# Kernel optimization log

Hardware: AMD Instinct MI355X
Metric: run time of the kernel (lower is better)

The kernel has to match this reference:

```python
import jax, jax.numpy as jnp
import numpy as np

B, H, W = 2, 224, 224
E, NH, DH, DFF = 64, 4, 16, 2048


def _conv2d(x, w, b):
    # stride-1 3x3 conv, padding=1 == SAME
    y = jax.lax.conv_general_dilated(x, w, (1, 1), 'SAME',
                                     dimension_numbers=('NCHW', 'OIHW', 'NCHW'))
    return y + b[None, :, None, None]


def _layer_norm(x, g, b, eps=1e-5):
    mu = x.mean(-1, keepdims=True)
    xc = x - mu
    var = (xc * xc).mean(-1, keepdims=True)
    return g * xc * jax.lax.rsqrt(var + eps) + b


def setup_inputs() -> dict:
    key = jax.random.key(0)
    ks = jax.random.split(key, 16)
    rn = lambda k, shape, s=0.05: jax.random.normal(k, shape, dtype=jnp.float32) * s
    z = lambda n: jnp.zeros((n,), jnp.float32)
    return {
        'x': jax.random.normal(ks[0], (B, 3, H, W), dtype=jnp.float32),
        'enc_w1': rn(ks[1], (64, 3, 3, 3)), 'enc_b1': z(64),
        'enc_w2': rn(ks[2], (64, 64, 3, 3)), 'enc_b2': z(64),
        'in_proj_w': rn(ks[3], (3 * E, E)), 'in_proj_b': z(3 * E),
        'out_proj_w': rn(ks[4], (E, E)), 'out_proj_b': z(E),
        'ln1_g': jnp.ones((E,), jnp.float32), 'ln1_b': z(E),
        'ffn_w1': rn(ks[5], (DFF, E)), 'ffn_b1': z(DFF),
        'ffn_w2': rn(ks[6], (E, DFF)), 'ffn_b2': z(E),
        'ln2_g': jnp.ones((E,), jnp.float32), 'ln2_b': z(E),
        'sf_w1': rn(ks[7], (32, 64, 3, 3)), 'sf_b1': z(32),
        'sf_w2': rn(ks[8], (9, 32, 3, 3)), 'sf_b2': z(9),
        'dec_w1': rn(ks[9], (64, 1, 3, 3)), 'dec_b1': z(64),
        'dec_w2': rn(ks[10], (1, 64, 3, 3)), 'dec_b2': z(1),
    }


def _forward(x, enc_w1, enc_b1, enc_w2, enc_b2,
             in_proj_w, in_proj_b, out_proj_w, out_proj_b,
             ln1_g, ln1_b, ffn_w1, ffn_b1, ffn_w2, ffn_b2, ln2_g, ln2_b,
             sf_w1, sf_b1, sf_w2, sf_b2, dec_w1, dec_b1, dec_w2, dec_b2):
    # ---- encoder ----
    e = jax.nn.relu(_conv2d(x, enc_w1, enc_b1))
    e = jax.nn.relu(_conv2d(e, enc_w2, enc_b2))
    b, c, h, w = e.shape
    # torch TransformerEncoderLayer default batch_first=False: [B, HW, E] is (S=B, N=HW, E)
    t = e.reshape(b, c, h * w).transpose(0, 2, 1)  # [S=B, N=HW, E]
    qkv = t @ in_proj_w.T + in_proj_b
    q, k, v = jnp.split(qkv, 3, axis=-1)
    S, N = q.shape[0], q.shape[1]
    q = q.reshape(S, N, NH, DH)
    k = k.reshape(S, N, NH, DH)
    v = v.reshape(S, N, NH, DH)
    scores = jnp.einsum('snhd,tnhd->nhst', q, k) / np.float32(np.sqrt(DH))
    attn = jnp.einsum('nhst,tnhd->snhd', jax.nn.softmax(scores, axis=-1), v)
    attn = attn.reshape(S, N, E) @ out_proj_w.T + out_proj_b
    t = _layer_norm(t + attn, ln1_g, ln1_b)
    ff = jax.nn.relu(t @ ffn_w1.T + ffn_b1) @ ffn_w2.T + ffn_b2
    t = _layer_norm(t + ff, ln2_g, ln2_b)
    enc2 = t.transpose(0, 2, 1).reshape(b, c, h, w)
    # ---- spatially adaptive per-pixel 3x3 filter (KPN-style) ----
    f = _conv2d(_conv2d(enc2, sf_w1, sf_b1), sf_w2, sf_b2)
    filters = f.reshape(b, 3, 3, h, w)  # per-pixel 3x3 kernel
    s = x.sum(axis=1)  # accumulate over the 3 input channels -> [B,H,W]
    sp = jnp.pad(s, ((0, 0), (1, 1), (1, 1)))
    patches = jnp.stack([sp[:, u:u + h, v:v + w] for u in range(3) for v in range(3)],
                        axis=1).reshape(b, 3, 3, h, w)
    fused = (filters * patches).sum(axis=(1, 2))[:, None]  # [B,1,H,W]
    # ---- decoder ----
    d = jax.nn.relu(_conv2d(fused, dec_w1, dec_b1))
    return jax.nn.sigmoid(_conv2d(d, dec_w2, dec_b2))


def reference(x, enc_w1, enc_b1, enc_w2, enc_b2,
              in_proj_w, in_proj_b, out_proj_w, out_proj_b,
              ln1_g, ln1_b, ffn_w1, ffn_b1, ffn_w2, ffn_b2, ln2_g, ln2_b,
              sf_w1, sf_b1, sf_w2, sf_b2, dec_w1, dec_b1, dec_w2, dec_b2):
    return _forward(x, enc_w1, enc_b1, enc_w2, enc_b2,
                    in_proj_w, in_proj_b, out_proj_w, out_proj_b,
                    ln1_g, ln1_b, ffn_w1, ffn_b1, ffn_w2, ffn_b2, ln2_g, ln2_b,
                    sf_w1, sf_b1, sf_w2, sf_b2, dec_w1, dec_b1, dec_w2, dec_b2)
```

## Files before the change

kernel.cpp:

```cpp
#include <hip/hip_runtime.h>
#include <hip/hip_bf16.h>
#include <cstddef>

#define HW   50176
#define NPIX 100352
#define IW   224

typedef unsigned short ushort_t;
typedef __attribute__((ext_vector_type(8))) short bf16x8;
typedef __attribute__((ext_vector_type(8))) unsigned short ushort8;
typedef __attribute__((ext_vector_type(4))) float f32x4;
typedef __attribute__((ext_vector_type(2))) _Float16 f16x2;
typedef __attribute__((ext_vector_type(8))) _Float16 f16x8;

__device__ inline ushort_t f2bf(float f) {
    __hip_bfloat16 h = __float2bfloat16(f);
    return __builtin_bit_cast(ushort_t, h);
}
__device__ inline float bf2f(ushort_t u) {
    return __uint_as_float(((unsigned)u) << 16);
}
__device__ inline bf16x8 ldg8(const ushort_t* p) {
    return *reinterpret_cast<const bf16x8*>(p);
}
__device__ inline void b2f8(const ushort_t* p, float* f) {
    ushort8 v = *reinterpret_cast<const ushort8*>(p);
#pragma unroll
    for (int i = 0; i < 8; i++) f[i] = bf2f(v[i]);
}
__device__ inline f16x2 pk16(float a, float b) {
    return __builtin_bit_cast(f16x2, __builtin_amdgcn_cvt_pkrtz(a, b));
}

__device__ inline void dma16(const ushort_t* g, ushort_t* l) {
    __builtin_amdgcn_global_load_lds(
        (const __attribute__((address_space(1))) void*)g,
        (__attribute__((address_space(3))) void*)l, 16, 0, 0);
}

__device__ void conv1_body(int gid, const float* __restrict__ x,
                           const float* __restrict__ w,
                           const float* __restrict__ bias,
                           ushort_t* __restrict__ out)
{
    int b = gid >= HW;
    int p = gid - b * HW;
    int y = p / IW, xx = p - y * IW;

    float v[27];
#pragma unroll
    for (int ci = 0; ci < 3; ci++) {
        const float* ip = x + ((size_t)(b * 3 + ci)) * HW;
#pragma unroll
        for (int t = 0; t < 9; t++) {
            int dy = t / 3 - 1, dx = t % 3 - 1;
            int yy = y + dy, xc = xx + dx;
            float tv = 0.f;
            if ((unsigned)yy < (unsigned)IW && (unsigned)xc < (unsigned)IW)
                tv = ip[yy * IW + xc];
            v[ci * 9 + t] = tv;
        }
    }
#pragma unroll
    for (int g = 0; g < 8; g++) {
        ushort8 o8;
#pragma unroll
        for (int i = 0; i < 8; i++) {
            int co = g * 8 + i;
            float a = bias[co];
            const float* wp = w + co * 27;
#pragma unroll
            for (int k = 0; k < 27; k++) a = fmaf(v[k], wp[k], a);
            o8[i] = f2bf(fmaxf(a, 0.f));
        }
        *reinterpret_cast<ushort8*>(out + (size_t)gid * 64 + g * 8) = o8;
    }
}

__global__ __launch_bounds__(256) void prep_conv1_k(
    const float* __restrict__ x,     const float* __restrict__ enc_w1,
    const float* __restrict__ enc_b1, ushort_t* __restrict__ E1b,
    const float* __restrict__ in_w,  ushort_t* __restrict__ in_wb,
    const float* __restrict__ out_w, ushort_t* __restrict__ out_wb,
    const float* __restrict__ w1,    ushort_t* __restrict__ w1p,
    const float* __restrict__ w2,    _Float16* __restrict__ w2s,
    const float* __restrict__ ec2,   ushort_t* __restrict__ wc2p,
    const float* __restrict__ s1,    ushort_t* __restrict__ ws1p,
    const float* __restrict__ s2,    ushort_t* __restrict__ ws2)
{
    if (blockIdx.x < 392) {
        conv1_body(blockIdx.x * 256 + threadIdx.x, x, enc_w1, enc_b1, E1b);
        return;
    }
    int idx = (blockIdx.x - 392) * 256 + threadIdx.x;
    if (idx < 12288) { in_wb[idx] = f2bf(in_w[idx]); return; }
    idx -= 12288;
    if (idx < 4096)  { out_wb[idx] = f2bf(out_w[idx]); return; }
    idx -= 4096;
    if (idx < 131072){
        int j = idx >> 6, e = idx & 63;
        int c = j >> 6, jl = j & 63;
        w1p[(size_t)c * 6144 + jl * 72 + e] = f2bf(w1[idx]);
        return;
    }
    idx -= 131072;
    if (idx < 131072){
        int j    = idx & 7;
        int lane = (idx >> 3) & 63;
        int rest = idx >> 9;
        int nt   = rest & 3;
        int cp   = rest >> 2;
        int p    = cp & 1;
        int c    = cp >> 1;
        int quad = lane >> 4;
        int e2   = nt * 16 + (lane & 15);
        int hl   = (j < 4) ? (quad * 4 + j) : (16 + quad * 4 + (j - 4));
        int hidden = c * 64 + p * 32 + hl;
        w2s[idx] = (_Float16)w2[(size_t)e2 * 2048 + hidden];
        return;
    }
    idx -= 131072;
    if (idx < 36864) {
        int ci = idx & 63, co = (idx >> 6) & 63, t = idx >> 12;
        wc2p[(size_t)t * 4608 + co * 72 + ci] = f2bf(ec2[((size_t)co * 64 + ci) * 9 + t]);
        return;
    }
    idx -= 36864;
    if (idx < 18432) {
        int ci = idx & 63, co = (idx >> 6) & 31, t = idx >> 11;
        ws1p[(size_t)t * 2560 + co * 72 + ci] = f2bf(s1[((size_t)co * 64 + ci) * 9 + t]);
        return;
    }
    idx -= 18432;
    if (idx < 4608)  {
        int ci = idx % 32;
        int t  = (idx / 32) % 9;
        int co = idx / 288;
        ws2[idx] = (co < 9) ? f2bf(s2[((size_t)co * 32 + ci) * 9 + t]) : (ushort_t)0;
        return;
    }
}

__global__ __launch_bounds__(256) void enc2xf_k(
    const ushort_t* __restrict__ E1b, const ushort_t* __restrict__ Wc2p,
    const float* __restrict__ enc_b2,
    const ushort_t* __restrict__ Wqkv, const float* __restrict__ Bqkv,
    const ushort_t* __restrict__ Wo, const float* __restrict__ Bo,
    const float* __restrict__ g, const float* __restrict__ be,
    ushort_t* __restrict__ T1b)
{
    __shared__ ushort_t Q[128 * 200];
    __shared__ ushort_t WT[9216];

    int tid = threadIdx.x, wave = tid >> 6, lane = tid & 63;
    int lm = lane & 15, quad = lane >> 4;
    int p0 = blockIdx.x * 64;

    {
        int lr0 = wave * 32;
        int m[2], py[2], px[2];
#pragma unroll
        for (int mt = 0; mt < 2; mt++) {
            int lr = lr0 + mt * 16 + lm;
            int gp = p0 + (lr & 63);
            m[mt] = (lr >> 6) * HW + gp;
            py[mt] = gp / IW;
            px[mt] = gp - py[mt] * IW;
        }

        f32x4 acc[2][4] = {};
        bf16x8 zz = {};

        auto dma_tap = [&](int t, int pb) {
            const ushort_t* gw = Wc2p + (size_t)t * 4608;
#pragma unroll
            for (int i = 0; i < 3; i++) {
                int idx = i * 4 + wave;
                if (idx < 9)
                    dma16(gw + idx * 512 + lane * 8, &WT[pb * 4608 + idx * 512]);
            }
        };

        dma_tap(0, 0);

        for (int t = 0; t < 9; t++) {
            int pb = t & 1;
            __syncthreads();
            if (t < 8) dma_tap(t + 1, pb ^ 1);

            int dy = t / 3 - 1, dx = t % 3 - 1;
            bf16x8 af[2][2];
#pragma unroll
            for (int mt = 0; mt < 2; mt++) {
                bool ok = (unsigned)(py[mt] + dy) < (unsigned)IW &&
                          (unsigned)(px[mt] + dx) < (unsigned)IW;
                const ushort_t* ip = E1b + (size_t)(m[mt] + dy * IW + dx) * 64 + quad * 8;
#pragma unroll
                for (int ks = 0; ks < 2; ks++)
                    af[mt][ks] = ok ? ldg8(ip + ks * 32) : zz;
            }
#pragma unroll
            for (int nt = 0; nt < 4; nt++) {
                const ushort_t* wp = &WT[pb * 4608 + (nt * 16 + lm) * 72 + quad * 8];
#pragma unroll
                for (int ks = 0; ks < 2; ks++) {
                    bf16x8 bfv = *reinterpret_cast<const bf16x8*>(wp + ks * 32);
#pragma unroll
                    for (int mt = 0; mt < 2; mt++)
                        acc[mt][nt] = __builtin_amdgcn_mfma_f32_16x16x32_bf16(
                            af[mt][ks], bfv, acc[mt][nt], 0, 0, 0);
                }
            }
        }

        __syncthreads();
#pragma unroll
        for (int nt = 0; nt < 4; nt++) {
            float bv = enc_b2[nt * 16 + lm];
#pragma unroll
            for (int mt = 0; mt < 2; mt++)
#pragma unroll
                for (int r = 0; r < 4; r++) {
                    int lr = lr0 + mt * 16 + quad * 4 + r;
                    WT[lr * 72 + nt * 16 + lm] =
                        f2bf(fmaxf(acc[mt][nt][r] + bv, 0.f));
                }
        }
    }
    __syncthreads();

#pragma unroll
    for (int mt = 0; mt < 2; mt++) {
        int lA = mt * 64 + wave * 16;
        bf16x8 a[2];
#pragma unroll
        for (int ks = 0; ks < 2; ks++)
            a[ks] = *reinterpret_cast<const bf16x8*>(
                &WT[(lA + lm) * 72 + ks * 32 + quad * 8]);
        f32x4 acc[12] = {};
#pragma unroll
        for (int nt = 0; nt < 12; nt++)
#pragma unroll
            for (int ks = 0; ks < 2; ks++) {
                bf16x8 b = ldg8(Wqkv + (size_t)(nt * 16 + lm) * 64 + ks * 32 + quad * 8);
                acc[nt] = __builtin_amdgcn_mfma_f32_16x16x32_bf16(a[ks], b, acc[nt], 0, 0, 0);
            }
        int lrow = lA + quad * 4;
#pragma unroll
        for (int nt = 0; nt < 12; nt++) {
            float bb = Bqkv[nt * 16 + lm];
#pragma unroll
            for (int r = 0; r < 4; r++)
                Q[(lrow + r) * 200 + nt * 16 + lm] = f2bf(acc[nt][r] + bb);
        }
    }
    __syncthreads();

    {
        int px = tid >> 2, h = tid & 3;
        ushort_t* r0 = &Q[px * 200 + h * 16];
        ushort_t* r1 = &Q[(64 + px) * 200 + h * 16];

        float q0[16], k0[16], v0[16], q1[16], k1[16], v1[16];
        b2f8(r0,       q0); b2f8(r0 + 8,   q0 + 8);
        b2f8(r0 + 64,  k0); b2f8(r0 + 72,  k0 + 8);
        b2f8(r0 + 128, v0); b2f8(r0 + 136, v0 + 8);
        b2f8(r1,       q1); b2f8(r1 + 8,   q1 + 8);
        b2f8(r1 + 64,  k1); b2f8(r1 + 72,  k1 + 8);
        b2f8(r1 + 128, v1); b2f8(r1 + 136, v1 + 8);

        float s00 = 0, s01 = 0, s10 = 0, s11 = 0;
#pragma unroll
        for (int d = 0; d < 16; d++) {
            s00 += q0[d] * k0[d]; s01 += q0[d] * k1[d];
            s10 += q1[d] * k0[d]; s11 += q1[d] * k1[d];
        }
        s00 *= 0.25f; s01 *= 0.25f; s10 *= 0.25f; s11 *= 0.25f;

        float m0 = fmaxf(s00, s01);
        float e00 = __expf(s00 - m0), e01 = __expf(s01 - m0);
        float i0 = 1.f / (e00 + e01);
        float p00 = e00 * i0, p01 = e01 * i0;

        float m1 = fmaxf(s10, s11);
        float e10 = __expf(s10 - m1), e11 = __expf(s11 - m1);
        float i1 = 1.f / (e10 + e11);
        float p10 = e10 * i1, p11 = e11 * i1;

#pragma unroll
        for (int c = 0; c < 2; c++) {
            ushort8 a0v, a1v;
#pragma unroll
            for (int i = 0; i < 8; i++) {
                int d = c * 8 + i;
                a0v[i] = f2bf(p00 * v0[d] + p01 * v1[d]);
                a1v[i] = f2bf(p10 * v0[d] + p11 * v1[d]);
            }
            *reinterpret_cast<ushort8*>(r0 + c * 8) = a0v;
            *reinterpret_cast<ushort8*>(r1 + c * 8) = a1v;
        }
    }
    __syncthreads();

#pragma unroll
    for (int mt = 0; mt < 2; mt++) {
        int lA = mt * 64 + wave * 16;
        size_t gbase = (size_t)((mt == 0 ? p0 : HW + p0) + wave * 16);
        bf16x8 a[2];
#pragma unroll
        for (int ks = 0; ks < 2; ks++)
            a[ks] = *reinterpret_cast<const bf16x8*>(
                &Q[(lA + lm) * 200 + ks * 32 + quad * 8]);
        f32x4 acc[4] = {};
#pragma unroll
        for (int nt = 0; nt < 4; nt++)
#pragma unroll
            for (int ks = 0; ks < 2; ks++) {
                bf16x8 b = ldg8(Wo + (size_t)(nt * 16 + lm) * 64 + ks * 32 + quad * 8);
                acc[nt] = __builtin_amdgcn_mfma_f32_16x16x32_bf16(a[ks], b, acc[nt], 0, 0, 0);
            }

        float bv[4], gv[4], bev[4];
#pragma unroll
        for (int nt = 0; nt < 4; nt++) {
            bv[nt]  = Bo[nt * 16 + lm];
            gv[nt]  = g[nt * 16 + lm];
            bev[nt] = be[nt * 16 + lm];
        }
#pragma unroll
        for (int r = 0; r < 4; r++) {
            int lr = lA + quad * 4 + r;
            size_t row = gbase + quad * 4 + r;
            float v[4]; float s = 0.f;
#pragma unroll
            for (int nt = 0; nt < 4; nt++) {
                v[nt] = acc[nt][r] + bv[nt] + bf2f(WT[lr * 72 + nt * 16 + lm]);
                s += v[nt];
            }
#pragma unroll
            for (int o = 8; o; o >>= 1) s += __shfl_xor(s, o, 64);
            float mu = s * 0.015625f;
            float q = 0.f;
#pragma unroll
            for (int nt = 0; nt < 4; nt++) { v[nt] -= mu; q += v[nt] * v[nt]; }
#pragma unroll
            for (int o = 8; o; o >>= 1) q += __shfl_xor(q, o, 64);
            float rstd = rsqrtf(q * 0.015625f + 1e-5f);
#pragma unroll
            for (int nt = 0; nt < 4; nt++)
                T1b[row * 64 + nt * 16 + lm] = f2bf(gv[nt] * v[nt] * rstd + bev[nt]);
        }
    }
}

template<int KS, int NT, int TAPUS, int NISSUE, int ACT, bool WF32, bool WB16>
__global__ __launch_bounds__(256) void neconv_lds_k(
    const ushort_t* __restrict__ In, const ushort_t* __restrict__ Wp,
    const float* __restrict__ bias, float* __restrict__ Of,
    ushort_t* __restrict__ Ob)
{
    const int CIN = KS * 32, LDO = NT * 16;
    __shared__ ushort_t Wl[2][TAPUS];

    int tid = threadIdx.x, wave = tid >> 6, lane = tid & 63;
    int lm = lane & 15, quad = lane >> 4;
    int m0 = blockIdx.x * 128 + wave * 32;

    int m[2], py[2], px[2];
#pragma unroll
    for (int mt = 0; mt < 2; mt++) {
        int mm = m0 + mt * 16 + lm;
        m[mt] = mm;
        int p = mm - (mm >= HW ? HW : 0);
        py[mt] = p / IW;
        px[mt] = p - py[mt] * IW;
    }

    f32x4 acc[2][NT] = {};
    bf16x8 zz = {};

    auto dma_tap = [&](int t, int pb) {
        const ushort_t* g = Wp + (size_t)t * TAPUS;
#pragma unroll
        for (int i = 0; i < (NISSUE + 3) / 4; i++) {
            int idx = i * 4 + wave;
            if (idx < NISSUE)
                dma16(g + idx * 512 + lane * 8, &Wl[pb][idx * 512]);
        }
    };

    dma_tap(0, 0);

    for (int t = 0; t < 9; t++) {
        int pb = t & 1;
        __syncthreads();
        if (t < 8) dma_tap(t + 1, pb ^ 1);

        int dy = t / 3 - 1, dx = t % 3 - 1;
        bf16x8 af[2][KS];
#pragma unroll
        for (int mt = 0; mt < 2; mt++) {
            bool ok = (unsigned)(py[mt] + dy) < (unsigned)IW &&
                      (unsigned)(px[mt] + dx) < (unsigned)IW;
            const ushort_t* ip = In + (size_t)(m[mt] + dy * IW + dx) * CIN + quad * 8;
#pragma unroll
            for (int ks = 0; ks < KS; ks++)
                af[mt][ks] = ok ? ldg8(ip + ks * 32) : zz;
        }
#pragma unroll
        for (int nt = 0; nt < NT; nt++) {
            const ushort_t* wp = &Wl[pb][(nt * 16 + lm) * 72 + quad * 8];
#pragma unroll
            for (int ks = 0; ks < KS; ks++) {
                bf16x8 bfv = *reinterpret_cast<const bf16x8*>(wp + ks * 32);
#pragma unroll
                for (int mt = 0; mt < 2; mt++)
                    acc[mt][nt] = __builtin_amdgcn_mfma_f32_16x16x32_bf16(
                        af[mt][ks], bfv, acc[mt][nt], 0, 0, 0);
            }
        }
    }

#pragma unroll
    for (int nt = 0; nt < NT; nt++) {
        int col = nt * 16 + lm;
        float bv = bias[col];
#pragma unroll
        for (int mt = 0; mt < 2; mt++)
#pragma unroll
            for (int r = 0; r < 4; r++) {
                int row = m0 + mt * 16 + quad * 4 + r;
                float v = acc[mt][nt][r] + bv;
                if (ACT) v = fmaxf(v, 0.f);
                if (WF32) Of[(size_t)row * LDO + col] = v;
                if (WB16) Ob[(size_t)row * LDO + col] = f2bf(v);
            }
    }
}

__global__ __launch_bounds__(512) void ffn9_k(
    const ushort_t* __restrict__ T1b,
    const ushort_t* __restrict__ W1p, const float* __restrict__ B1,
    const _Float16* __restrict__ W2s, const float* __restrict__ B2,
    const float* __restrict__ g, const float* __restrict__ be,
    ushort_t* __restrict__ OutTb)
{
    __shared__ ushort_t W1lds[3][6144];
    __shared__ ushort_t W2lds[3][4096];
    __shared__ float    B1l[2048];

    int tid = threadIdx.x, wave = tid >> 6, lane = tid & 63;
    int lm = lane & 15, quad = lane >> 4;
    int rowbase = blockIdx.x * 256 + wave * 32;

    *reinterpret_cast<float4*>(&B1l[tid * 4]) =
        *reinterpret_cast<const float4*>(B1 + tid * 4);

    bf16x8 Bt[2][2];
#pragma unroll
    for (int mt = 0; mt < 2; mt++)
#pragma unroll
        for (int ks = 0; ks < 2; ks++)
            Bt[mt][ks] = ldg8(T1b + (size_t)(rowbase + mt * 16 + lm) * 64 + ks * 32 + quad * 8);

    __syncthreads();

    auto dma_chunk = [&](int c, int pb) {
        const ushort_t* g1 = W1p + (size_t)c * 6144;
        const ushort_t* g2 = (const ushort_t*)(W2s + (size_t)c * 4096);
#pragma unroll
        for (int i = 0; i < 3; i++) {
            int idx = i * 8 + wave;
            if (idx < 12)
                dma16(g1 + idx * 512 + lane * 8, &W1lds[pb][idx * 512]);
            else if (idx < 20)
                dma16(g2 + (idx - 12) * 512 + lane * 8,
                      &W2lds[pb][(idx - 12) * 512]);
        }
    };

    dma_chunk(0, 0);
    dma_chunk(1, 1);

    f32x4 acc[2][4] = {};

    for (int c = 0; c < 32; c++) {
        int pb = c % 3;

        if (c < 31) {
            if (wave < 4) asm volatile("s_waitcnt vmcnt(3)" ::: "memory");
            else          asm volatile("s_waitcnt vmcnt(2)" ::: "memory");
        } else {
            asm volatile("s_waitcnt vmcnt(0)" ::: "memory");
        }
        __builtin_amdgcn_s_barrier();
        asm volatile("" ::: "memory");

        if (c + 2 < 32) dma_chunk(c + 2, (c + 2) % 3);

        const ushort_t* w1l = &W1lds[pb][0];
        const ushort_t* w2l = &W2lds[pb][0];

#pragma unroll
        for (int p = 0; p < 2; p++) {
            bf16x8 w1r[2][2];
            f16x8  w2r[4];
            float4 b1r[2];
#pragma unroll
            for (int s = 0; s < 2; s++) {
                int ul = p * 2 + s;
#pragma unroll
                for (int ks = 0; ks < 2; ks++)
                    w1r[s][ks] = *reinterpret_cast<const bf16x8*>(
                        &w1l[(ul * 16 + lm) * 72 + ks * 32 + quad * 8]);
                b1r[s] = *reinterpret_cast<const float4*>(
                    &B1l[(c * 4 + ul) * 16 + quad * 4]);
            }
#pragma unroll
            for (int nt = 0; nt < 4; nt++)
                w2r[nt] = *reinterpret_cast<const f16x8*>(
                    &w2l[((p * 4 + nt) * 64 + lane) * 8]);

            f32x4 h[2][2];
#pragma unroll
            for (int s = 0; s < 2; s++) {
                f32x4 binit = {b1r[s].x, b1r[s].y, b1r[s].z, b1r[s].w};
#pragma unroll
                for (int mt = 0; mt < 2; mt++) h[s][mt] = binit;
            }

            __builtin_amdgcn_s_setprio(1);
#pragma unroll
            for (int s = 0; s < 2; s++)
#pragma unroll
                for (int ks = 0; ks < 2; ks++)
#pragma unroll
                    for (int mt = 0; mt < 2; mt++)
                        h[s][mt] = __builtin_amdgcn_mfma_f32_16x16x32_bf16(
                            w1r[s][ks], Bt[mt][ks], h[s][mt], 0, 0, 0);

            f16x8 aH[2];
#pragma unroll
            for (int mt = 0; mt < 2; mt++) {
                f16x2 t0 = pk16(fmaxf(h[0][mt][0], 0.f), fmaxf(h[0][mt][1], 0.f));
                f16x2 t1 = pk16(fmaxf(h[0][mt][2], 0.f), fmaxf(h[0][mt][3], 0.f));
                f16x2 t2 = pk16(fmaxf(h[1][mt][0], 0.f), fmaxf(h[1][mt][1], 0.f));
                f16x2 t3 = pk16(fmaxf(h[1][mt][2], 0.f), fmaxf(h[1][mt][3], 0.f));
                f16x8 a;
                a[0] = t0[0]; a[1] = t0[1]; a[2] = t1[0]; a[3] = t1[1];
                a[4] = t2[0]; a[5] = t2[1]; a[6] = t3[0]; a[7] = t3[1];
                aH[mt] = a;
            }

#pragma unroll
            for (int nt = 0; nt < 4; nt++)
#pragma unroll
                for (int mt = 0; mt < 2; mt++)
                    acc[mt][nt] = __builtin_amdgcn_mfma_f32_16x16x32_f16(
                        aH[mt], w2r[nt], acc[mt][nt], 0, 0, 0);
            __builtin_amdgcn_s_setprio(0);
        }
    }

    float b2v[4], gv[4], bev[4];
#pragma unroll
    for (int nt = 0; nt < 4; nt++) {
        b2v[nt] = B2[nt * 16 + lm];
        gv[nt]  = g[nt * 16 + lm];
        bev[nt] = be[nt * 16 + lm];
    }
#pragma unroll
    for (int mt = 0; mt < 2; mt++)
#pragma unroll
        for (int r = 0; r < 4; r++) {
            int row = rowbase + mt * 16 + quad * 4 + r;
            float v[4]; float s = 0.f;
#pragma unroll
            for (int nt = 0; nt < 4; nt++) {
                v[nt] = acc[mt][nt][r] + b2v[nt] +
                        bf2f(T1b[(size_t)row * 64 + nt * 16 + lm]);
                s += v[nt];
            }
#pragma unroll
            for (int o = 8; o; o >>= 1) s += __shfl_xor(s, o, 64);
            float mu = s * 0.015625f;
            float q = 0.f;
#pragma unroll
            for (int nt = 0; nt < 4; nt++) { v[nt] -= mu; q += v[nt] * v[nt]; }
#pragma unroll
            for (int o = 8; o; o >>= 1) q += __shfl_xor(q, o, 64);
            float rstd = rsqrtf(q * 0.015625f + 1e-5f);
#pragma unroll
            for (int nt = 0; nt < 4; nt++)
                OutTb[(size_t)row * 64 + nt * 16 + lm] =
                    f2bf(gv[nt] * v[nt] * rstd + bev[nt]);
        }
}

__global__ __launch_bounds__(256) void sf2kpn_k(
    const ushort_t* __restrict__ In,
    const ushort_t* __restrict__ Wsw,
    const float* __restrict__ bias,
    const float* __restrict__ x,
    float* __restrict__ fused)
{
    __shared__ float Fl[128 * 12];
    int tid = threadIdx.x, wave = tid >> 6, lane = tid & 63;
    int lm = lane & 15, quad = lane >> 4;
    int m0 = blockIdx.x * 128 + wave * 32;

    int m[2], py[2], px[2];
#pragma unroll
    for (int mt = 0; mt < 2; mt++) {
        int mm = m0 + mt * 16 + lm;
        m[mt] = mm;
        int p = mm - (mm >= HW ? HW : 0);
        py[mt] = p / IW;
        px[mt] = p - py[mt] * IW;
    }

    f32x4 acc[2] = {};
    bf16x8 zz = {};

#pragma unroll 3
    for (int t = 0; t < 9; t++) {
        int dy = t / 3 - 1, dx = t % 3 - 1;
        bf16x8 af[2];
#pragma unroll
        for (int mt = 0; mt < 2; mt++) {
            bool ok = (unsigned)(py[mt] + dy) < (unsigned)IW &&
                      (unsigned)(px[mt] + dx) < (unsigned)IW;
            af[mt] = ok ? ldg8(In + (size_t)(m[mt] + dy * IW + dx) * 32 + quad * 8) : zz;
        }
        bf16x8 bfv = ldg8(Wsw + ((size_t)lm * 9 + t) * 32 + quad * 8);
#pragma unroll
        for (int mt = 0; mt < 2; mt++)
            acc[mt] = __builtin_amdgcn_mfma_f32_16x16x32_bf16(af[mt], bfv, acc[mt], 0, 0, 0);
    }

    if (lm < 9) {
        float bv = bias[lm];
#pragma unroll
        for (int mt = 0; mt < 2; mt++)
#pragma unroll
            for (int r = 0; r < 4; r++) {
                int lrow = wave * 32 + mt * 16 + quad * 4 + r;
                Fl[lrow * 12 + lm] = acc[mt][r] + bv;
            }
    }
    __syncthreads();

    if (tid < 128) {
        int gid = blockIdx.x * 128 + tid;
        int b = gid >= HW;
        int p = gid - b * HW;
        int y = p / IW, xx = p - y * IW;
        const float* fp = &Fl[tid * 12];
        const float* xp = x + (size_t)b * 3 * HW;
        float a = 0.f;
#pragma unroll
        for (int u = 0; u < 3; u++) {
            int yy = y + u - 1;
            if ((unsigned)yy >= (unsigned)IW) continue;
#pragma unroll
            for (int v = 0; v < 3; v++) {
                int xc = xx + v - 1;
                if ((unsigned)xc >= (unsigned)IW) continue;
                int o = yy * IW + xc;
                float s = xp[o] + xp[HW + o] + xp[2 * HW + o];
                a += fp[u * 3 + v] * s;
            }
        }
        fused[gid] = a;
    }
}

__global__ __launch_bounds__(256) void dec_fused_k(
    const float* __restrict__ fused,
    const float* __restrict__ w1, const float* __restrict__ b1,
    const float* __restrict__ w2, const float* __restrict__ b2,
    float* __restrict__ out)
{
    int gid = blockIdx.x * 256 + threadIdx.x;
    int b = gid >= HW;
    int p = gid - b * HW;
    int y = p / IW, xx = p - y * IW;
    const float* ip = fused + (size_t)b * HW;

    float F[25];
#pragma unroll
    for (int u = 0; u < 5; u++)
#pragma unroll
        for (int v = 0; v < 5; v++) {
            int yy = y + u - 2, xc = xx + v - 2;
            float t = 0.f;
            if ((unsigned)yy < (unsigned)IW && (unsigned)xc < (unsigned)IW)
                t = ip[yy * IW + xc];
            F[u * 5 + v] = t;
        }
    float nm[9];
#pragma unroll
    for (int n = 0; n < 9; n++) {
        int yy = y + n / 3 - 1, xc = xx + n % 3 - 1;
        nm[n] = ((unsigned)yy < (unsigned)IW && (unsigned)xc < (unsigned)IW) ? 1.f : 0.f;
    }

    float acc = b2[0];
    for (int c = 0; c < 64; c++) {
        float w1c[9], w2c[9];
#pragma unroll
        for (int s = 0; s < 9; s++) { w1c[s] = w1[c * 9 + s]; w2c[s] = w2[c * 9 + s]; }
        float bc = b1[c];
#pragma unroll
        for (int n = 0; n < 9; n++) {
            int ny = n / 3, nx0 = n % 3;
            float h = bc;
#pragma unroll
            for (int s = 0; s < 9; s++)
                h = fmaf(F[(ny + s / 3) * 5 + (nx0 + s % 3)], w1c[s], h);
            acc = fmaf(fmaxf(h, 0.f), w2c[n] * nm[n], acc);
        }
    }
    out[gid] = 1.f / (1.f + __expf(-acc));
}

extern "C" void kernel_launch(void* const* d_in, const int* in_sizes, int n_in,
                              void* d_out, int out_size, void* d_ws, size_t ws_size,
                              hipStream_t stream)
{
    const float* x      = (const float*)d_in[0];
    const float* enc_w1 = (const float*)d_in[1];
    const float* enc_b1 = (const float*)d_in[2];
    const float* enc_w2 = (const float*)d_in[3];
    const float* enc_b2 = (const float*)d_in[4];
    const float* in_w   = (const float*)d_in[5];
    const float* in_b   = (const float*)d_in[6];
    const float* out_w  = (const float*)d_in[7];
    const float* out_b  = (const float*)d_in[8];
    const float* ln1_g  = (const float*)d_in[9];
    const float* ln1_b  = (const float*)d_in[10];
    const float* ffn_w1 = (const float*)d_in[11];
    const float* ffn_b1 = (const float*)d_in[12];
    const float* ffn_w2 = (const float*)d_in[13];
    const float* ffn_b2 = (const float*)d_in[14];
    const float* ln2_g  = (const float*)d_in[15];
    const float* ln2_b  = (const float*)d_in[16];
    const float* sf_w1  = (const float*)d_in[17];
    const float* sf_b1  = (const float*)d_in[18];
    const float* sf_w2  = (const float*)d_in[19];
    const float* sf_b2  = (const float*)d_in[20];
    const float* dec_w1 = (const float*)d_in[21];
    const float* dec_b1 = (const float*)d_in[22];
    const float* dec_w2 = (const float*)d_in[23];
    const float* dec_b2 = (const float*)d_in[24];

    float* ws = (float*)d_ws;
    const size_t SZ = (size_t)NPIX * 64;

    ushort_t* E1b  = (ushort_t*)(ws + 5 * SZ);
    ushort_t* Tb   = (ushort_t*)(ws + 11 * SZ / 2);
    ushort_t* wu   = (ushort_t*)(ws + 6 * SZ);
    ushort_t* in_wb  = wu;
    ushort_t* out_wb = wu + 12288;
    ushort_t* w1p    = wu + 16384;
    _Float16* w2s    = (_Float16*)(wu + 212992);
    ushort_t* wc2p   = wu + 344064;
    ushort_t* ws1p   = wu + 385536;
    ushort_t* ws2    = wu + 408576;
    float*    base3 = ws + 3 * SZ;
    ushort_t* s1b   = (ushort_t*)base3;
    float*    fused = base3 + SZ / 2;

    prep_conv1_k<<<1714, 256, 0, stream>>>(
        x, enc_w1, enc_b1, E1b,
        in_w, in_wb, out_w, out_wb, ffn_w1, w1p,
        ffn_w2, w2s, enc_w2, wc2p, sf_w1, ws1p, sf_w2, ws2);

    enc2xf_k<<<784, 256, 0, stream>>>(E1b, wc2p, enc_b2,
                                      in_wb, in_b, out_wb, out_b,
                                      ln1_g, ln1_b, Tb);
    ffn9_k<<<392, 512, 0, stream>>>(Tb, w1p, ffn_b1, w2s, ffn_b2, ln2_g, ln2_b, E1b);
    neconv_lds_k<2, 2, 2560, 5, 0, false, true><<<784, 256, 0, stream>>>(
        E1b, ws1p, sf_b1, nullptr, s1b);
    sf2kpn_k<<<784, 256, 0, stream>>>(s1b, ws2, sf_b2, x, fused);
    dec_fused_k<<<392, 256, 0, stream>>>(fused, dec_w1, dec_b1, dec_w2, dec_b2,
                                         (float*)d_out);
}
```

Baseline: 309.0 us.

## Split fused decoder into two kernels with fp16 intermediate to avoid 9x recompute

The fused decoder kernel recomputed the 64-channel first conv at all 9 neighbor positions for each output pixel, about 9x redundant FLOPs. It is now split into dec1_k, which computes the 64 ReLU activations once per pixel and stores them as fp16, and dec2_k, which reads the 9 neighbor vectors and applies the second conv. This trades compute for about 13 MB of extra global traffic plus one more launch, and adds fp16 rounding of the intermediate.

```diff
diff --git a/kernel.cpp b/kernel.cpp
--- a/kernel.cpp
+++ b/kernel.cpp
@@ -675,9 +675,45 @@
     }
 }
 
-__global__ __launch_bounds__(256) void dec_fused_k(
+__global__ __launch_bounds__(256) void dec1_k(
     const float* __restrict__ fused,
     const float* __restrict__ w1, const float* __restrict__ b1,
+    _Float16* __restrict__ Hb)
+{
+    int gid = blockIdx.x * 256 + threadIdx.x;
+    int b = gid >= HW;
+    int p = gid - b * HW;
+    int y = p / IW, xx = p - y * IW;
+    const float* ip = fused + (size_t)b * HW;
+
+    float F[9];
+#pragma unroll
+    for (int s = 0; s < 9; s++) {
+        int yy = y + s / 3 - 1, xc = xx + s % 3 - 1;
+        float t = 0.f;
+        if ((unsigned)yy < (unsigned)IW && (unsigned)xc < (unsigned)IW)
+            t = ip[yy * IW + xc];
+        F[s] = t;
+    }
+    _Float16* op = Hb + (size_t)gid * 64;
+#pragma unroll
+    for (int g = 0; g < 8; g++) {
+        f16x8 o;
+#pragma unroll
+        for (int i = 0; i < 8; i++) {
+            int c = g * 8 + i;
+            float h = b1[c];
+            const float* wp = w1 + c * 9;
+#pragma unroll
+            for (int s = 0; s < 9; s++) h = fmaf(F[s], wp[s], h);
+            o[i] = (_Float16)fmaxf(h, 0.f);
+        }
+        *reinterpret_cast<f16x8*>(op + g * 8) = o;
+    }
+}
+
+__global__ __launch_bounds__(256) void dec2_k(
+    const _Float16* __restrict__ Hb,
     const float* __restrict__ w2, const float* __restrict__ b2,
     float* __restrict__ out)
 {
@@ -685,40 +721,21 @@
     int b = gid >= HW;
     int p = gid - b * HW;
     int y = p / IW, xx = p - y * IW;
-    const float* ip = fused + (size_t)b * HW;
-
-    float F[25];
-#pragma unroll
-    for (int u = 0; u < 5; u++)
-#pragma unroll
-        for (int v = 0; v < 5; v++) {
-            int yy = y + u - 2, xc = xx + v - 2;
-            float t = 0.f;
-            if ((unsigned)yy < (unsigned)IW && (unsigned)xc < (unsigned)IW)
-                t = ip[yy * IW + xc];
-            F[u * 5 + v] = t;
-        }
-    float nm[9];
+    (void)b;
+
+    float acc = b2[0];
 #pragma unroll
     for (int n = 0; n < 9; n++) {
-        int yy = y + n / 3 - 1, xc = xx + n % 3 - 1;
-        nm[n] = ((unsigned)yy < (unsigned)IW && (unsigned)xc < (unsigned)IW) ? 1.f : 0.f;
-    }
-
-    float acc = b2[0];
-    for (int c = 0; c < 64; c++) {
-        float w1c[9], w2c[9];
-#pragma unroll
-        for (int s = 0; s < 9; s++) { w1c[s] = w1[c * 9 + s]; w2c[s] = w2[c * 9 + s]; }
-        float bc = b1[c];
-#pragma unroll
-        for (int n = 0; n < 9; n++) {
-            int ny = n / 3, nx0 = n % 3;
-            float h = bc;
-#pragma unroll
-            for (int s = 0; s < 9; s++)
-                h = fmaf(F[(ny + s / 3) * 5 + (nx0 + s % 3)], w1c[s], h);
-            acc = fmaf(fmaxf(h, 0.f), w2c[n] * nm[n], acc);
+        int dy = n / 3 - 1, dx = n % 3 - 1;
+        int yy = y + dy, xc = xx + dx;
+        if ((unsigned)yy >= (unsigned)IW || (unsigned)xc >= (unsigned)IW) continue;
+        const _Float16* hp = Hb + (size_t)(gid + dy * IW + dx) * 64;
+#pragma unroll
+        for (int g = 0; g < 8; g++) {
+            f16x8 hv = *reinterpret_cast<const f16x8*>(hp + g * 8);
+#pragma unroll
+            for (int i = 0; i < 8; i++)
+                acc = fmaf((float)hv[i], w2[(g * 8 + i) * 9 + n], acc);
         }
     }
     out[gid] = 1.f / (1.f + __expf(-acc));
@@ -770,6 +787,7 @@
     float*    base3 = ws + 3 * SZ;
     ushort_t* s1b   = (ushort_t*)base3;
     float*    fused = base3 + SZ / 2;
+    _Float16* Hb    = (_Float16*)(ws + 4 * SZ);
 
     prep_conv1_k<<<1714, 256, 0, stream>>>(
         x, enc_w1, enc_b1, E1b,
@@ -783,6 +801,6 @@
     neconv_lds_k<2, 2, 2560, 5, 0, false, true><<<784, 256, 0, stream>>>(
         E1b, ws1p, sf_b1, nullptr, s1b);
     sf2kpn_k<<<784, 256, 0, stream>>>(s1b, ws2, sf_b2, x, fused);
-    dec_fused_k<<<392, 256, 0, stream>>>(fused, dec_w1, dec_b1, dec_w2, dec_b2,
-                                         (float*)d_out);
-}
+    dec1_k<<<392, 256, 0, stream>>>(fused, dec_w1, dec_b1, Hb);
+    dec2_k<<<392, 256, 0, stream>>>(Hb, dec_w2, dec_b2, (float*)d_out);
+}
```

Measured after the change: 313.4 us. About the same (+1.4%).
